# Performance work log

Hardware: AMD Instinct MI355X
Metric: run time of the kernel (lower is better)

The kernel has to match this reference:

```python
import jax, jax.numpy as jnp
import numpy as np

IN_F, OUT_F, N_CH, N_TILES, PTS = 256, 256, 1024, 1024, 256
OMEGA = 30.0


def setup_inputs() -> dict:
    key = jax.random.key(0)
    kx, kw, kb, ki = jax.random.split(key, 4)
    bound = float(np.sqrt(6.0 / IN_F) / OMEGA)  # SIREN-style init (is_first=False)
    x = jax.random.normal(kx, (N_TILES, PTS, IN_F), dtype=jnp.float32)
    weight = jax.random.uniform(kw, (N_CH, IN_F, OUT_F), dtype=jnp.float32,
                                minval=-bound, maxval=bound)
    bias = jax.random.uniform(kb, (1, 1, OUT_F), dtype=jnp.float32,
                              minval=-bound, maxval=bound)
    indices = jax.random.randint(ki, (N_TILES,), 0, N_CH, dtype=jnp.int64)
    return {"x": x, "weight": weight, "bias": bias, "indices": indices}


def reference(x, weight, bias, indices):
    # gather per-tile weight slice then batched matmul: [T,P,I] @ [T,I,O] -> [T,P,O]
    w = weight[indices]                      # [T, I, O]
    out = jnp.einsum('tpi,tio->tpo', x, w) + bias[0]
    return jnp.sin(OMEGA * out)
```

## Files before the change

kernel.cpp:

```cpp
#include <hip/hip_runtime.h>

typedef _Float16 half8_t __attribute__((ext_vector_type(8)));
typedef _Float16 half4_t __attribute__((ext_vector_type(4)));
typedef float    float4_t __attribute__((ext_vector_type(4)));

#define N_TILES 1024
#define PTS     256
#define IN_F    256
#define OUT_F   256
#define BK      32
#define LDK     40
#define NSTEP   (IN_F / BK)
#define OMEGA_C 30.0f

__global__ __launch_bounds__(512, 2)
void siren_tile_gemm(const float* __restrict__ x,
                     const float* __restrict__ w,
                     const float* __restrict__ bias,
                     const void* __restrict__ idx_raw,
                     float* __restrict__ out) {
  __shared__ __align__(16) _Float16 Al[2][PTS][LDK];
  __shared__ __align__(16) _Float16 Bl[2][OUT_F][LDK];
  __shared__ int s_is32;

  const int tid  = threadIdx.x;
  const int tile = blockIdx.x;

  if (tid == 0) s_is32 = 0;
  __syncthreads();
  if (((const int*)idx_raw)[2 * tid + 1] != 0) atomicOr(&s_is32, 1);
  __syncthreads();
  const int ch = s_is32 ? ((const int*)idx_raw)[tile]
                        : (int)(((const long long*)idx_raw)[tile]);

  const float* __restrict__ Xg = x + (size_t)tile * (PTS * IN_F);
  const float* __restrict__ Wg = w + (size_t)ch * (IN_F * OUT_F);

  const int a_row = tid >> 3;
  const int a_lir = tid & 7;
  const int b_kb = tid >> 6;
  const int b_nb = tid & 63;

  float4_t acc[8][4];
#pragma unroll
  for (int m = 0; m < 8; ++m)
#pragma unroll
    for (int n = 0; n < 4; ++n)
      acc[m][n] = (float4_t){0.f, 0.f, 0.f, 0.f};

  float4_t a_ld[4], b_ld[4];

#pragma unroll
  for (int p = 0; p < 4; ++p)
    a_ld[p] = *(const float4_t*)(Xg + (size_t)(a_row + 64 * p) * IN_F + a_lir * 4);
#pragma unroll
  for (int j = 0; j < 4; ++j)
    b_ld[j] = *(const float4_t*)(Wg + (size_t)(b_kb * 4 + j) * OUT_F + b_nb * 4);
#pragma unroll
  for (int p = 0; p < 4; ++p) {
    half4_t h = {(_Float16)a_ld[p].x, (_Float16)a_ld[p].y,
                 (_Float16)a_ld[p].z, (_Float16)a_ld[p].w};
    *(half4_t*)&Al[0][a_row + 64 * p][a_lir * 4] = h;
  }
#pragma unroll
  for (int i = 0; i < 4; ++i) {
    half4_t h = {(_Float16)b_ld[0][i], (_Float16)b_ld[1][i],
                 (_Float16)b_ld[2][i], (_Float16)b_ld[3][i]};
    *(half4_t*)&Bl[0][b_nb * 4 + i][b_kb * 4] = h;
  }
  __syncthreads();

  const int wid  = tid >> 6;
  const int lane = tid & 63;
  const int mrow = (wid >> 2) * 128;
  const int ncol = (wid & 3) * 64;
  const int fr   = lane & 15;
  const int kg   = lane >> 4;

#pragma unroll 2
  for (int s = 0; s < NSTEP; ++s) {
    const int cur = s & 1;
    if (s + 1 < NSTEP) {
      const int k0 = (s + 1) * BK;
#pragma unroll
      for (int p = 0; p < 4; ++p)
        a_ld[p] = *(const float4_t*)(Xg + (size_t)(a_row + 64 * p) * IN_F + k0 + a_lir * 4);
#pragma unroll
      for (int j = 0; j < 4; ++j)
        b_ld[j] = *(const float4_t*)(Wg + (size_t)(k0 + b_kb * 4 + j) * OUT_F + b_nb * 4);
    }

    half8_t af[8], bf[4];
#pragma unroll
    for (int m = 0; m < 8; ++m)
      af[m] = *(const half8_t*)&Al[cur][mrow + m * 16 + fr][kg * 8];
#pragma unroll
    for (int n = 0; n < 4; ++n)
      bf[n] = *(const half8_t*)&Bl[cur][ncol + n * 16 + fr][kg * 8];

#pragma unroll
    for (int m = 0; m < 8; ++m)
#pragma unroll
      for (int n = 0; n < 4; ++n)
        acc[m][n] = __builtin_amdgcn_mfma_f32_16x16x32_f16(af[m], bf[n], acc[m][n], 0, 0, 0);

    if (s + 1 < NSTEP) {
      const int nxt = cur ^ 1;
#pragma unroll
      for (int p = 0; p < 4; ++p) {
        half4_t h = {(_Float16)a_ld[p].x, (_Float16)a_ld[p].y,
                     (_Float16)a_ld[p].z, (_Float16)a_ld[p].w};
        *(half4_t*)&Al[nxt][a_row + 64 * p][a_lir * 4] = h;
      }
#pragma unroll
      for (int i = 0; i < 4; ++i) {
        half4_t h = {(_Float16)b_ld[0][i], (_Float16)b_ld[1][i],
                     (_Float16)b_ld[2][i], (_Float16)b_ld[3][i]};
        *(half4_t*)&Bl[nxt][b_nb * 4 + i][b_kb * 4] = h;
      }
    }
    __syncthreads();
  }

  float bv[4];
#pragma unroll
  for (int n = 0; n < 4; ++n) bv[n] = bias[ncol + n * 16 + fr];

  float* __restrict__ Og = out + (size_t)tile * (PTS * OUT_F);
#pragma unroll
  for (int m = 0; m < 8; ++m) {
#pragma unroll
    for (int n = 0; n < 4; ++n) {
#pragma unroll
      for (int j = 0; j < 4; ++j) {
        const int row = mrow + m * 16 + kg * 4 + j;
        const int col = ncol + n * 16 + fr;
        Og[(size_t)row * OUT_F + col] = __sinf(OMEGA_C * (acc[m][n][j] + bv[n]));
      }
    }
  }
}

extern "C" void kernel_launch(void* const* d_in, const int* in_sizes, int n_in,
                              void* d_out, int out_size, void* d_ws, size_t ws_size,
                              hipStream_t stream) {
  const float* x    = (const float*)d_in[0];
  const float* w    = (const float*)d_in[1];
  const float* bias = (const float*)d_in[2];
  const void*  idx  = d_in[3];
  float*       out  = (float*)d_out;

  siren_tile_gemm<<<N_TILES, 512, 0, stream>>>(x, w, bias, idx, out);
}
```

Before: 158.9 us.

## Split each tile into two M-halves with XCD-aware mapping and swizzled B LDS

Each tile is now processed by two blocks that each own 128 rows, doubling the grid and halving the per-block accumulator and A staging, with occupancy raised to four blocks per CU. Block IDs are remapped so the two halves of a tile land on the same XCD, so the shared weight slice stays in that XCD's L2. The B tile in LDS gets an XOR swizzle to cut bank conflicts on fragment reads. The weight prefetch moves after the MFMA block behind a sched_barrier, the index-width check uses a wave vote instead of shared atomics, and bias is pre-scaled into an fma. The weight slice is now read twice per tile, and the launch-bounds change tightens the register budget.

Result: no change. 160.0 us (+0.7%).

```diff
diff --git a/kernel.cpp b/kernel.cpp
--- a/kernel.cpp
+++ b/kernel.cpp
@@ -8,72 +8,79 @@
 #define PTS     256
 #define IN_F    256
 #define OUT_F   256
+#define BM      128
 #define BK      32
 #define LDK     40
 #define NSTEP   (IN_F / BK)
 #define OMEGA_C 30.0f
 
-__global__ __launch_bounds__(512, 2)
+__global__ __launch_bounds__(512, 4)
 void siren_tile_gemm(const float* __restrict__ x,
                      const float* __restrict__ w,
                      const float* __restrict__ bias,
                      const void* __restrict__ idx_raw,
                      float* __restrict__ out) {
-  __shared__ __align__(16) _Float16 Al[2][PTS][LDK];
+  __shared__ __align__(16) _Float16 Al[2][BM][LDK];
   __shared__ __align__(16) _Float16 Bl[2][OUT_F][LDK];
-  __shared__ int s_is32;
 
-  const int tid  = threadIdx.x;
-  const int tile = blockIdx.x;
+  const int tid = threadIdx.x;
 
-  if (tid == 0) s_is32 = 0;
-  __syncthreads();
-  if (((const int*)idx_raw)[2 * tid + 1] != 0) atomicOr(&s_is32, 1);
-  __syncthreads();
-  const int ch = s_is32 ? ((const int*)idx_raw)[tile]
-                        : (int)(((const long long*)idx_raw)[tile]);
+  const int s_id = blockIdx.x;
+  const int xcd  = s_id & 7;
+  const int k_id = s_id >> 3;
+  const int tile = xcd + 8 * (k_id >> 1);
+  const int mh   = k_id & 1;
 
-  const float* __restrict__ Xg = x + (size_t)tile * (PTS * IN_F);
+  const int hiw  = ((const int*)idx_raw)[2 * (tid & 63) + 1];
+  const bool is32 = __any(hiw != 0);
+  const int ch = is32 ? ((const int*)idx_raw)[tile]
+                      : (int)(((const long long*)idx_raw)[tile]);
+
+  const float* __restrict__ Xg = x + (size_t)tile * (PTS * IN_F) + (size_t)mh * BM * IN_F;
   const float* __restrict__ Wg = w + (size_t)ch * (IN_F * OUT_F);
+  float*       __restrict__ Og = out + (size_t)tile * (PTS * OUT_F) + (size_t)mh * BM * OUT_F;
 
   const int a_row = tid >> 3;
   const int a_lir = tid & 7;
-  const int b_kb = tid >> 6;
-  const int b_nb = tid & 63;
+  const int b_kb  = tid >> 6;
+  const int b_nb  = tid & 63;
 
-  float4_t acc[8][4];
+  float4_t acc[4][4];
 #pragma unroll
-  for (int m = 0; m < 8; ++m)
+  for (int m = 0; m < 4; ++m)
 #pragma unroll
     for (int n = 0; n < 4; ++n)
       acc[m][n] = (float4_t){0.f, 0.f, 0.f, 0.f};
 
-  float4_t a_ld[4], b_ld[4];
+  float4_t a_ld[2], b_ld[4];
+
+#define BSWZ(g, n) (((g) ^ (((n) >> 3) & 3)))
 
 #pragma unroll
-  for (int p = 0; p < 4; ++p)
+  for (int p = 0; p < 2; ++p)
     a_ld[p] = *(const float4_t*)(Xg + (size_t)(a_row + 64 * p) * IN_F + a_lir * 4);
 #pragma unroll
   for (int j = 0; j < 4; ++j)
     b_ld[j] = *(const float4_t*)(Wg + (size_t)(b_kb * 4 + j) * OUT_F + b_nb * 4);
 #pragma unroll
-  for (int p = 0; p < 4; ++p) {
+  for (int p = 0; p < 2; ++p) {
     half4_t h = {(_Float16)a_ld[p].x, (_Float16)a_ld[p].y,
                  (_Float16)a_ld[p].z, (_Float16)a_ld[p].w};
     *(half4_t*)&Al[0][a_row + 64 * p][a_lir * 4] = h;
   }
 #pragma unroll
   for (int i = 0; i < 4; ++i) {
+    const int n = b_nb * 4 + i;
     half4_t h = {(_Float16)b_ld[0][i], (_Float16)b_ld[1][i],
                  (_Float16)b_ld[2][i], (_Float16)b_ld[3][i]};
-    *(half4_t*)&Bl[0][b_nb * 4 + i][b_kb * 4] = h;
+    *(half4_t*)&Bl[0][n][BSWZ(b_kb >> 1, n) * 8 + (b_kb & 1) * 4] = h;
   }
   __syncthreads();
 
+  const int lane = tid & 63;
   const int wid  = tid >> 6;
-  const int lane = tid & 63;
-  const int mrow = (wid >> 2) * 128;
-  const int ncol = (wid & 3) * 64;
+  const int wm   = (wid >> 2) * 64;
+  const int wn   = (wid & 3) * 64;
   const int fr   = lane & 15;
   const int kg   = lane >> 4;
 
@@ -83,59 +90,64 @@
     if (s + 1 < NSTEP) {
       const int k0 = (s + 1) * BK;
 #pragma unroll
-      for (int p = 0; p < 4; ++p)
+      for (int p = 0; p < 2; ++p)
         a_ld[p] = *(const float4_t*)(Xg + (size_t)(a_row + 64 * p) * IN_F + k0 + a_lir * 4);
-#pragma unroll
-      for (int j = 0; j < 4; ++j)
-        b_ld[j] = *(const float4_t*)(Wg + (size_t)(k0 + b_kb * 4 + j) * OUT_F + b_nb * 4);
     }
 
-    half8_t af[8], bf[4];
+    half8_t af[4], bf[4];
 #pragma unroll
-    for (int m = 0; m < 8; ++m)
-      af[m] = *(const half8_t*)&Al[cur][mrow + m * 16 + fr][kg * 8];
+    for (int m = 0; m < 4; ++m)
+      af[m] = *(const half8_t*)&Al[cur][wm + m * 16 + fr][kg * 8];
 #pragma unroll
-    for (int n = 0; n < 4; ++n)
-      bf[n] = *(const half8_t*)&Bl[cur][ncol + n * 16 + fr][kg * 8];
+    for (int n = 0; n < 4; ++n) {
+      const int r = wn + n * 16 + fr;
+      bf[n] = *(const half8_t*)&Bl[cur][r][BSWZ(kg, r) * 8];
+    }
 
 #pragma unroll
-    for (int m = 0; m < 8; ++m)
+    for (int m = 0; m < 4; ++m)
 #pragma unroll
       for (int n = 0; n < 4; ++n)
         acc[m][n] = __builtin_amdgcn_mfma_f32_16x16x32_f16(af[m], bf[n], acc[m][n], 0, 0, 0);
 
+    __builtin_amdgcn_sched_barrier(0);
+
     if (s + 1 < NSTEP) {
+      const int k0 = (s + 1) * BK;
       const int nxt = cur ^ 1;
 #pragma unroll
-      for (int p = 0; p < 4; ++p) {
+      for (int j = 0; j < 4; ++j)
+        b_ld[j] = *(const float4_t*)(Wg + (size_t)(k0 + b_kb * 4 + j) * OUT_F + b_nb * 4);
+#pragma unroll
+      for (int p = 0; p < 2; ++p) {
         half4_t h = {(_Float16)a_ld[p].x, (_Float16)a_ld[p].y,
                      (_Float16)a_ld[p].z, (_Float16)a_ld[p].w};
         *(half4_t*)&Al[nxt][a_row + 64 * p][a_lir * 4] = h;
       }
 #pragma unroll
       for (int i = 0; i < 4; ++i) {
+        const int n = b_nb * 4 + i;
         half4_t h = {(_Float16)b_ld[0][i], (_Float16)b_ld[1][i],
                      (_Float16)b_ld[2][i], (_Float16)b_ld[3][i]};
-        *(half4_t*)&Bl[nxt][b_nb * 4 + i][b_kb * 4] = h;
+        *(half4_t*)&Bl[nxt][n][BSWZ(b_kb >> 1, n) * 8 + (b_kb & 1) * 4] = h;
       }
+      __syncthreads();
     }
-    __syncthreads();
   }
 
   float bv[4];
 #pragma unroll
-  for (int n = 0; n < 4; ++n) bv[n] = bias[ncol + n * 16 + fr];
+  for (int n = 0; n < 4; ++n) bv[n] = OMEGA_C * bias[wn + n * 16 + fr];
 
-  float* __restrict__ Og = out + (size_t)tile * (PTS * OUT_F);
 #pragma unroll
-  for (int m = 0; m < 8; ++m) {
+  for (int m = 0; m < 4; ++m) {
 #pragma unroll
     for (int n = 0; n < 4; ++n) {
 #pragma unroll
       for (int j = 0; j < 4; ++j) {
-        const int row = mrow + m * 16 + kg * 4 + j;
-        const int col = ncol + n * 16 + fr;
-        Og[(size_t)row * OUT_F + col] = __sinf(OMEGA_C * (acc[m][n][j] + bv[n]));
+        const int row = wm + m * 16 + kg * 4 + j;
+        const int col = wn + n * 16 + fr;
+        Og[(size_t)row * OUT_F + col] = __sinf(fmaf(OMEGA_C, acc[m][n][j], bv[n]));
       }
     }
   }
@@ -150,5 +162,5 @@
   const void*  idx  = d_in[3];
   float*       out  = (float*)d_out;
 
-  siren_tile_gemm<<<N_TILES, 512, 0, stream>>>(x, w, bias, idx, out);
+  siren_tile_gemm<<<N_TILES * 2, 512, 0, stream>>>(x, w, bias, idx, out);
 }
```
